# Kernel optimization log

Measured on AMD Instinct MI355X. Metric: run time of the kernel, lower is better.

The kernel has to match this reference:

```python
import jax, jax.numpy as jnp
import numpy as np

DIM = 1024
NUM_ROT = 1024
BATCH = 65536


def setup_inputs() -> dict:
    key = jax.random.key(0)
    k1, k2 = jax.random.split(key)
    x = jax.random.normal(k1, (BATCH, DIM), dtype=jnp.float32)
    angles = jax.random.normal(k2, (NUM_ROT,), dtype=jnp.float32)
    return {"x": x, "angles": angles}


def reference(x, angles):
    # Sequential Givens rotations. out @ R.T with R[i,i]=R[j,j]=c, R[i,j]=-s, R[j,i]=s
    # is equivalent to: col_i' = c*col_i - s*col_j ; col_j' = s*col_i + c*col_j.
    dim = x.shape[-1]
    num_rot = angles.shape[0]
    ii = jnp.arange(num_rot, dtype=jnp.int32)          # pairs (i, (i+1)%dim)
    jj = (ii + 1) % dim

    def step(out, inp):
        theta, i, j = inp
        c, s = jnp.cos(theta), jnp.sin(theta)
        ci = out[:, i]
        cj = out[:, j]
        out = out.at[:, i].set(c * ci - s * cj)
        out = out.at[:, j].set(s * ci + c * cj)
        return out, None

    out, _ = jax.lax.scan(step, x, (angles, ii, jj))
    return out
```

## Files before the change

kernel.cpp:

```cpp
#include <hip/hip_runtime.h>

#define DIM   1024
#define LPR   32
#define SEG   (DIM / LPR)
#define SEG4  (SEG / 4)
#define ROWS_PER_BLOCK 8
#define WAVES_PER_BLOCK 4

typedef float f32x4 __attribute__((ext_vector_type(4)));

__global__ __launch_bounds__(256, 4)
void qll_kernel(const float* __restrict__ x,
                const float* __restrict__ angles,
                float* __restrict__ out,
                int batch)
{
    __shared__ float2 cs[DIM];
    __shared__ f32x4  stage[WAVES_PER_BLOCK][512];

    const int tid  = threadIdx.x;
    const int l    = tid & 63;
    const int wave = tid >> 6;
    const int h    = (tid >> 5) & 1;
    const int t    = tid & 31;
    const int r0   = blockIdx.x * ROWS_PER_BLOCK + wave * 2;
    const bool active = (r0 + 2 <= batch);

    const int swz_l = l ^ ((l >> 3) & 7);

    const f32x4* gin = reinterpret_cast<const f32x4*>(x) + (size_t)r0 * 256;
    if (active) {
#pragma unroll
        for (int m = 0; m < 8; ++m) {
            __builtin_amdgcn_global_load_lds(
                (const __attribute__((address_space(1))) void*)(gin + m * 64 + swz_l),
                (__attribute__((address_space(3))) void*)(&stage[wave][m * 64]),
                16, 0, 0);
        }
    }

    for (int loc = tid; loc < DIM; loc += 256) {
        int j = ((loc & 31) << 5) | (loc >> 5);
        float a = angles[j];
        cs[loc] = make_float2(cosf(a), sinf(a));
    }
    __syncthreads();
    if (!active) return;
    asm volatile("s_waitcnt vmcnt(0)" ::: "memory");
    __builtin_amdgcn_sched_barrier(0);

    float v[SEG];
#pragma unroll
    for (int e = 0; e < SEG4; ++e) {
        f32x4 q = stage[wave][h * 256 + t * 8 + (e ^ (t & 7))];
        v[4*e+0] = q.x; v[4*e+1] = q.y; v[4*e+2] = q.z; v[4*e+3] = q.w;
    }

    float v0row = __shfl(v[0], 0, LPR);
    float v1row = __shfl(v[1], 0, LPR);
    float vnext = __shfl_down(v[0], 1, LPR);

    float A = 1.f, B = 0.f;
#pragma unroll
    for (int i = 0; i < SEG - 1; ++i) {
        float2 w = cs[i * LPR + t];
        B = w.y * B + w.x * v[i + 1];
        A = w.y * A;
    }
    {
        float2 w = cs[(SEG - 1) * LPR + t];
        B = w.y * B + w.x * vnext;
        A = w.y * A;
    }

#pragma unroll
    for (int d = 1; d < LPR; d <<= 1) {
        float pa = __shfl_up(A, d, LPR);
        float pb = __shfl_up(B, d, LPR);
        if (t >= d) { B = A * pb + B; A = A * pa; }
    }
    float ea = __shfl_up(A, 1, LPR);
    float eb = __shfl_up(B, 1, LPR);
    if (t == 0) { ea = 1.f; eb = 0.f; }
    float carry = ea * v0row + eb;

    float2 w0 = cs[0];
    float out0_prov = w0.x * v0row - w0.y * v1row;

#pragma unroll
    for (int i = 0; i < SEG - 1; ++i) {
        float2 w = cs[i * LPR + t];
        float vn = v[i + 1];
        float o  = w.x * carry - w.y * vn;
        carry    = w.y * carry + w.x * vn;
        v[i] = o;
    }
    {
        float2 w  = cs[(SEG - 1) * LPR + t];
        float vn  = (t == LPR - 1) ? out0_prov : vnext;
        float o   = w.x * carry - w.y * vn;
        float nc  = w.y * carry + w.x * vn;
        v[SEG - 1] = o;
        float out0_final = __shfl(nc, LPR - 1, LPR);
        if (t == 0) v[0] = out0_final;
    }

#pragma unroll
    for (int e = 0; e < SEG4; ++e) {
        f32x4 q = { v[4*e+0], v[4*e+1], v[4*e+2], v[4*e+3] };
        stage[wave][h * 256 + t * 8 + (e ^ (t & 7))] = q;
    }
    f32x4* gout = reinterpret_cast<f32x4*>(out) + (size_t)r0 * 256;
#pragma unroll
    for (int m = 0; m < 8; ++m) {
        f32x4 q = stage[wave][m * 64 + swz_l];
        __builtin_nontemporal_store(q, gout + m * 64 + l);
    }
}

extern "C" void kernel_launch(void* const* d_in, const int* in_sizes, int n_in,
                              void* d_out, int out_size, void* d_ws, size_t ws_size,
                              hipStream_t stream) {
    const float* x      = (const float*)d_in[0];
    const float* angles = (const float*)d_in[1];
    float* outp         = (float*)d_out;

    int batch = in_sizes[0] / DIM;
    int grid  = (batch + ROWS_PER_BLOCK - 1) / ROWS_PER_BLOCK;
    qll_kernel<<<grid, 256, 0, stream>>>(x, angles, outp, batch);
}
```

Measured before the change: 102.8 us.

## Precompute cos/sin table in a prelaunch kernel and stream it into LDS

A small kernel now computes the transposed cos/sin table into the workspace once. The main kernel copies that table into LDS with async global-to-LDS loads, instead of every block evaluating cosf/sinf for 1024 angles, and it uses a raw s_barrier with a partial vmcnt wait. This removes per-block transcendental work and overlaps the table fetch with the row loads, at the cost of an extra launch. A fallback kernel keeps the old behaviour when no workspace is available.

```diff
diff --git a/kernel.cpp b/kernel.cpp
--- a/kernel.cpp
+++ b/kernel.cpp
@@ -8,10 +8,20 @@
 #define WAVES_PER_BLOCK 4
 
 typedef float f32x4 __attribute__((ext_vector_type(4)));
+#define AS1 __attribute__((address_space(1)))
+#define AS3 __attribute__((address_space(3)))
+
+__global__ void qll_table(const float* __restrict__ angles, float2* __restrict__ ws) {
+    int j = blockIdx.x * blockDim.x + threadIdx.x;
+    if (j < DIM) {
+        float a = angles[j];
+        ws[(j & 31) * LPR + (j >> 5)] = make_float2(cosf(a), sinf(a));
+    }
+}
 
 __global__ __launch_bounds__(256, 4)
 void qll_kernel(const float* __restrict__ x,
-                const float* __restrict__ angles,
+                const float2* __restrict__ csws,
                 float* __restrict__ out,
                 int batch)
 {
@@ -25,27 +35,29 @@
     const int t    = tid & 31;
     const int r0   = blockIdx.x * ROWS_PER_BLOCK + wave * 2;
     const bool active = (r0 + 2 <= batch);
+    const int rr   = active ? r0 : 0;
 
     const int swz_l = l ^ ((l >> 3) & 7);
 
-    const f32x4* gin = reinterpret_cast<const f32x4*>(x) + (size_t)r0 * 256;
-    if (active) {
-#pragma unroll
-        for (int m = 0; m < 8; ++m) {
-            __builtin_amdgcn_global_load_lds(
-                (const __attribute__((address_space(1))) void*)(gin + m * 64 + swz_l),
-                (__attribute__((address_space(3))) void*)(&stage[wave][m * 64]),
-                16, 0, 0);
-        }
-    }
-
-    for (int loc = tid; loc < DIM; loc += 256) {
-        int j = ((loc & 31) << 5) | (loc >> 5);
-        float a = angles[j];
-        cs[loc] = make_float2(cosf(a), sinf(a));
-    }
-    __syncthreads();
+    const f32x4* w4 = reinterpret_cast<const f32x4*>(csws);
+    f32x4* c4 = reinterpret_cast<f32x4*>(cs);
+    __builtin_amdgcn_global_load_lds((const AS1 void*)(w4 + wave * 64 + l),
+                                     (AS3 void*)(c4 + wave * 64), 16, 0, 0);
+    __builtin_amdgcn_global_load_lds((const AS1 void*)(w4 + 256 + wave * 64 + l),
+                                     (AS3 void*)(c4 + 256 + wave * 64), 16, 0, 0);
+
+    const f32x4* gin = reinterpret_cast<const f32x4*>(x) + (size_t)rr * 256;
+#pragma unroll
+    for (int m = 0; m < 8; ++m) {
+        __builtin_amdgcn_global_load_lds(
+            (const AS1 void*)(gin + m * 64 + swz_l),
+            (AS3 void*)(&stage[wave][m * 64]), 16, 0, 0);
+    }
+
+    asm volatile("s_waitcnt vmcnt(8)" ::: "memory");
+    __builtin_amdgcn_s_barrier();
     if (!active) return;
+
     asm volatile("s_waitcnt vmcnt(0)" ::: "memory");
     __builtin_amdgcn_sched_barrier(0);
 
@@ -118,6 +130,108 @@
     }
 }
 
+__global__ __launch_bounds__(256, 4)
+void qll_kernel_fb(const float* __restrict__ x,
+                   const float* __restrict__ angles,
+                   float* __restrict__ out,
+                   int batch)
+{
+    __shared__ float2 cs[DIM];
+    __shared__ f32x4  stage[WAVES_PER_BLOCK][512];
+
+    const int tid  = threadIdx.x;
+    const int l    = tid & 63;
+    const int wave = tid >> 6;
+    const int h    = (tid >> 5) & 1;
+    const int t    = tid & 31;
+    const int r0   = blockIdx.x * ROWS_PER_BLOCK + wave * 2;
+    const bool active = (r0 + 2 <= batch);
+    const int swz_l = l ^ ((l >> 3) & 7);
+
+    for (int loc = tid; loc < DIM; loc += 256) {
+        int j = ((loc & 31) << 5) | (loc >> 5);
+        float a = angles[j];
+        cs[loc] = make_float2(cosf(a), sinf(a));
+    }
+    __syncthreads();
+    if (!active) return;
+
+    const f32x4* gin = reinterpret_cast<const f32x4*>(x) + (size_t)r0 * 256;
+#pragma unroll
+    for (int m = 0; m < 8; ++m) {
+        __builtin_amdgcn_global_load_lds(
+            (const AS1 void*)(gin + m * 64 + swz_l),
+            (AS3 void*)(&stage[wave][m * 64]), 16, 0, 0);
+    }
+    asm volatile("s_waitcnt vmcnt(0)" ::: "memory");
+    __builtin_amdgcn_sched_barrier(0);
+
+    float v[SEG];
+#pragma unroll
+    for (int e = 0; e < SEG4; ++e) {
+        f32x4 q = stage[wave][h * 256 + t * 8 + (e ^ (t & 7))];
+        v[4*e+0] = q.x; v[4*e+1] = q.y; v[4*e+2] = q.z; v[4*e+3] = q.w;
+    }
+    float v0row = __shfl(v[0], 0, LPR);
+    float v1row = __shfl(v[1], 0, LPR);
+    float vnext = __shfl_down(v[0], 1, LPR);
+
+    float A = 1.f, B = 0.f;
+#pragma unroll
+    for (int i = 0; i < SEG - 1; ++i) {
+        float2 w = cs[i * LPR + t];
+        B = w.y * B + w.x * v[i + 1];
+        A = w.y * A;
+    }
+    {
+        float2 w = cs[(SEG - 1) * LPR + t];
+        B = w.y * B + w.x * vnext;
+        A = w.y * A;
+    }
+#pragma unroll
+    for (int d = 1; d < LPR; d <<= 1) {
+        float pa = __shfl_up(A, d, LPR);
+        float pb = __shfl_up(B, d, LPR);
+        if (t >= d) { B = A * pb + B; A = A * pa; }
+    }
+    float ea = __shfl_up(A, 1, LPR);
+    float eb = __shfl_up(B, 1, LPR);
+    if (t == 0) { ea = 1.f; eb = 0.f; }
+    float carry = ea * v0row + eb;
+
+    float2 w0 = cs[0];
+    float out0_prov = w0.x * v0row - w0.y * v1row;
+
+#pragma unroll
+    for (int i = 0; i < SEG - 1; ++i) {
+        float2 w = cs[i * LPR + t];
+        float vn = v[i + 1];
+        float o  = w.x * carry - w.y * vn;
+        carry    = w.y * carry + w.x * vn;
+        v[i] = o;
+    }
+    {
+        float2 w  = cs[(SEG - 1) * LPR + t];
+        float vn  = (t == LPR - 1) ? out0_prov : vnext;
+        float o   = w.x * carry - w.y * vn;
+        float nc  = w.y * carry + w.x * vn;
+        v[SEG - 1] = o;
+        float out0_final = __shfl(nc, LPR - 1, LPR);
+        if (t == 0) v[0] = out0_final;
+    }
+#pragma unroll
+    for (int e = 0; e < SEG4; ++e) {
+        f32x4 q = { v[4*e+0], v[4*e+1], v[4*e+2], v[4*e+3] };
+        stage[wave][h * 256 + t * 8 + (e ^ (t & 7))] = q;
+    }
+    f32x4* gout = reinterpret_cast<f32x4*>(out) + (size_t)r0 * 256;
+#pragma unroll
+    for (int m = 0; m < 8; ++m) {
+        f32x4 q = stage[wave][m * 64 + swz_l];
+        __builtin_nontemporal_store(q, gout + m * 64 + l);
+    }
+}
+
 extern "C" void kernel_launch(void* const* d_in, const int* in_sizes, int n_in,
                               void* d_out, int out_size, void* d_ws, size_t ws_size,
                               hipStream_t stream) {
@@ -127,5 +241,12 @@
 
     int batch = in_sizes[0] / DIM;
     int grid  = (batch + ROWS_PER_BLOCK - 1) / ROWS_PER_BLOCK;
-    qll_kernel<<<grid, 256, 0, stream>>>(x, angles, outp, batch);
-}
+
+    if (ws_size >= (size_t)(DIM * sizeof(float2))) {
+        float2* ws = (float2*)d_ws;
+        qll_table<<<(DIM + 255) / 256, 256, 0, stream>>>(angles, ws);
+        qll_kernel<<<grid, 256, 0, stream>>>(x, ws, outp, batch);
+    } else {
+        qll_kernel_fb<<<grid, 256, 0, stream>>>(x, angles, outp, batch);
+    }
+}
```

After: 90.84 us. 1.13x faster.
